# Optimization experiments

Measured on AMD Instinct MI355X. Metric: run time of the kernel, lower is better.

## Reference

```python
import jax, jax.numpy as jnp
import numpy as np

N = 3072      # packed vision tokens (multiple of _BLOCK=128, so no padding needed)
D = 1280      # hidden_size
H = 16        # num_heads
K = 80        # head_dim = D // H
NSEG = 8      # number of packed images/segments


def setup_inputs() -> dict:
    key = jax.random.key(0)
    ks = jax.random.split(key, 8)
    hidden_ND = jax.random.normal(ks[0], (N, D), jnp.float32)
    inner = jnp.sort(jax.random.randint(ks[1], (NSEG - 1,), 1, N)).astype(jnp.int32)
    cu_seqlens = jnp.concatenate([
        jnp.zeros((1,), jnp.int32), inner, jnp.full((1,), N, jnp.int32)])
    theta = jax.random.uniform(ks[2], (N, K), jnp.float32, 0.0, 2.0 * np.pi)
    cos_NK = jnp.cos(theta)
    sin_NK = jnp.sin(theta)
    sd = 1.0 / np.sqrt(D)  # lecun_normal-ish scale
    qkv_w = jax.random.normal(ks[3], (D, 3 * D), jnp.float32) * sd
    qkv_b = jax.random.normal(ks[4], (3 * D,), jnp.float32) * 0.01
    proj_w = jax.random.normal(ks[5], (D, D), jnp.float32) * sd
    proj_b = jax.random.normal(ks[6], (D,), jnp.float32) * 0.01
    return {"hidden_ND": hidden_ND, "cu_seqlens": cu_seqlens,
            "cos_NK": cos_NK, "sin_NK": sin_NK,
            "qkv_w": qkv_w, "qkv_b": qkv_b,
            "proj_w": proj_w, "proj_b": proj_b}


def _rotate_half(x):
    x1, x2 = jnp.split(x, 2, axis=-1)
    return jnp.concatenate([-x2, x1], axis=-1)


def _apply_vision_rope(q_NHK, k_NHK, cos_NK, sin_NK):
    c = cos_NK[:, None, :]  # (N, 1, K) broadcast over heads
    s = sin_NK[:, None, :]
    q = q_NHK * c + _rotate_half(q_NHK) * s
    k = k_NHK * c + _rotate_half(k_NHK) * s
    return q, k


def reference(hidden_ND, cu_seqlens, cos_NK, sin_NK, qkv_w, qkv_b, proj_w, proj_b):
    n = hidden_ND.shape[0]
    scale = K ** (-0.5)
    qkv = (hidden_ND @ qkv_w + qkv_b).reshape(n, 3, H, K)
    q_NHK, k_NHK, v_NHK = qkv[:, 0], qkv[:, 1], qkv[:, 2]
    q_NHK, k_NHK = _apply_vision_rope(q_NHK, k_NHK, cos_NK, sin_NK)

    # segment-boundary mask: token i attends to [k_start[i], k_end[i])
    idx = jnp.arange(n)
    seg = jnp.searchsorted(cu_seqlens[1:], idx, side='right')
    nseg = cu_seqlens.shape[0]
    k_start = cu_seqlens[jnp.minimum(seg, nseg - 2)]
    k_end = cu_seqlens[jnp.minimum(seg + 1, nseg - 1)]
    mask = (idx[None, :] >= k_start[:, None]) & (idx[None, :] < k_end[:, None])  # (Nq, Nk)

    scores = jnp.einsum('nhk,mhk->hnm', q_NHK, k_NHK) * scale  # (H, N, N)
    scores = jnp.where(mask[None], scores, jnp.float32(-1e30))
    probs = jax.nn.softmax(scores, axis=-1)
    attn = jnp.einsum('hnm,mhk->nhk', probs, v_NHK)  # (N, H, K)
    out_ND = attn.reshape(n, H * K) @ proj_w + proj_b
    return out_ND
```

## Files before the change

### kernel.cpp

```cpp
#include <hip/hip_runtime.h>

#define NTOK 3072
#define DM   1280
#define NH   16
#define HD   80
#define HDS  104
#define KVB  64
#define NSEG 8
#define QKVC 3840

typedef __attribute__((ext_vector_type(4))) float  f32x4;
typedef __attribute__((ext_vector_type(8))) __bf16 bf16x8;
typedef __attribute__((ext_vector_type(8))) unsigned short ushort8;
typedef __attribute__((ext_vector_type(4))) unsigned short ushort4v;
typedef __attribute__((ext_vector_type(2))) unsigned int  u32x2;

static __device__ __forceinline__ unsigned short f2bf(float f){
  union{float f; unsigned int u;} v; v.f=f;
  unsigned int r = v.u + 0x7fffu + ((v.u>>16)&1u);
  return (unsigned short)(r>>16);
}
static __device__ __forceinline__ float bf2f(unsigned short u){
  union{unsigned int i; float f;} v; v.i = ((unsigned int)u)<<16; return v.f;
}
static __device__ __forceinline__ void gload_lds16(const void* g, void* l){
  __builtin_amdgcn_global_load_lds((const __attribute__((address_space(1))) void*)g,
                                   (__attribute__((address_space(3))) void*)l, 16, 0, 0);
}

__global__ void cast_f32_bf16(const float* __restrict__ src, unsigned short* __restrict__ dst, int n){
  int i = (blockIdx.x*256 + threadIdx.x)*4;
  if (i >= n) return;
  f32x4 v = *reinterpret_cast<const f32x4*>(&src[i]);
  ushort4v o;
  o[0]=f2bf(v[0]); o[1]=f2bf(v[1]); o[2]=f2bf(v[2]); o[3]=f2bf(v[3]);
  *reinterpret_cast<ushort4v*>(&dst[i]) = o;
}

__global__ void transpose_cast(const float* __restrict__ src, unsigned short* __restrict__ dst, int R, int C){
  __shared__ unsigned short tile[32][33];
  int c0 = blockIdx.x*32, r0 = blockIdx.y*32;
  int tx = threadIdx.x, ty = threadIdx.y;
  #pragma unroll
  for (int i=0;i<4;i++){
    int r = r0 + ty + i*8;
    tile[ty+i*8][tx] = f2bf(src[(size_t)r*C + c0 + tx]);
  }
  __syncthreads();
  #pragma unroll
  for (int i=0;i<4;i++){
    int c = c0 + ty + i*8;
    dst[(size_t)c*R + r0 + tx] = tile[tx][ty+i*8];
  }
}

__global__ void transpose_v(const unsigned short* __restrict__ qkv, unsigned short* __restrict__ Vt){
  __shared__ unsigned short tile[32][33];
  int n0 = blockIdx.x*32, d0 = blockIdx.y*32, h = blockIdx.z;
  int tx = threadIdx.x, ty = threadIdx.y;
  #pragma unroll
  for (int i=0;i<4;i++){
    int n = n0 + ty + i*8;
    int d = d0 + tx;
    tile[ty+i*8][tx] = (d < HD) ? qkv[(size_t)n*QKVC + 2*DM + h*HD + d] : (unsigned short)0;
  }
  __syncthreads();
  #pragma unroll
  for (int i=0;i<4;i++){
    int d = d0 + ty + i*8;
    if (d < HD) Vt[((size_t)h*HD + d)*NTOK + n0 + tx] = tile[tx][ty+i*8];
  }
}

template<int OUT_BF16>
__global__ __launch_bounds__(256) void gemm_bt(
    const unsigned short* __restrict__ A,
    const unsigned short* __restrict__ Bt,
    const float* __restrict__ bias,
    unsigned short* __restrict__ Cb,
    float* __restrict__ Cf,
    int M, int Ncol, int Kd, int nbn)
{
  __shared__ unsigned short As[2][128*32];
  __shared__ unsigned short Bs[2][128*32];
  const int tid  = threadIdx.x;
  const int lane = tid & 63, wave = tid >> 6;
  const int wr = wave >> 1, wc = wave & 1;
  const int cpx = gridDim.x >> 3;
  const int id  = (blockIdx.x & 7)*cpx + (blockIdx.x >> 3);
  const int bm = id / nbn, bn = id % nbn;
  const f32x4 vzero = {0.f,0.f,0.f,0.f};

  f32x4 acc[4][4];
  #pragma unroll
  for (int i=0;i<4;i++)
    #pragma unroll
    for (int j=0;j<4;j++) acc[i][j] = vzero;

  const int rsub = lane>>2;
  const int kc   = (lane&3)*8;
  const unsigned short* Ab = A  + (size_t)(bm*128 + wave*32 + rsub)*Kd + kc;
  const unsigned short* Bb = Bt + (size_t)(bn*128 + wave*32 + rsub)*Kd + kc;

  #pragma unroll
  for (int i=0;i<2;i++){
    gload_lds16(Ab + (size_t)i*16*Kd, &As[0][(wave*2+i)*512]);
    gload_lds16(Bb + (size_t)i*16*Kd, &Bs[0][(wave*2+i)*512]);
  }
  __syncthreads();

  int cur = 0;
  for (int k0=32; k0<Kd; k0+=32){
    #pragma unroll
    for (int i=0;i<2;i++){
      gload_lds16(Ab + (size_t)i*16*Kd + k0, &As[cur^1][(wave*2+i)*512]);
      gload_lds16(Bb + (size_t)i*16*Kd + k0, &Bs[cur^1][(wave*2+i)*512]);
    }
    bf16x8 a[4], b[4];
    #pragma unroll
    for (int mf=0; mf<4; mf++)
      a[mf] = *reinterpret_cast<const bf16x8*>(&As[cur][(wr*64 + mf*16 + (lane&15))*32 + ((lane>>4)<<3)]);
    #pragma unroll
    for (int nf=0; nf<4; nf++)
      b[nf] = *reinterpret_cast<const bf16x8*>(&Bs[cur][(wc*64 + nf*16 + (lane&15))*32 + ((lane>>4)<<3)]);
    #pragma unroll
    for (int mf=0; mf<4; mf++)
      #pragma unroll
      for (int nf=0; nf<4; nf++)
        acc[mf][nf] = __builtin_amdgcn_mfma_f32_16x16x32_bf16(a[mf], b[nf], acc[mf][nf], 0,0,0);
    __syncthreads();
    cur ^= 1;
  }
  {
    bf16x8 a[4], b[4];
    #pragma unroll
    for (int mf=0; mf<4; mf++)
      a[mf] = *reinterpret_cast<const bf16x8*>(&As[cur][(wr*64 + mf*16 + (lane&15))*32 + ((lane>>4)<<3)]);
    #pragma unroll
    for (int nf=0; nf<4; nf++)
      b[nf] = *reinterpret_cast<const bf16x8*>(&Bs[cur][(wc*64 + nf*16 + (lane&15))*32 + ((lane>>4)<<3)]);
    #pragma unroll
    for (int mf=0; mf<4; mf++)
      #pragma unroll
      for (int nf=0; nf<4; nf++)
        acc[mf][nf] = __builtin_amdgcn_mfma_f32_16x16x32_bf16(a[mf], b[nf], acc[mf][nf], 0,0,0);
  }

  const int crow0 = bm*128 + wr*64;
  const int ccol0 = bn*128 + wc*64;
  #pragma unroll
  for (int nf=0; nf<4; nf++){
    int col = ccol0 + nf*16 + (lane&15);
    float bv = bias[col];
    #pragma unroll
    for (int mf=0; mf<4; mf++){
      #pragma unroll
      for (int r=0;r<4;r++){
        int row = crow0 + mf*16 + ((lane>>4)<<2) + r;
        float v = acc[mf][nf][r] + bv;
        if (OUT_BF16) Cb[(size_t)row*Ncol + col] = f2bf(v);
        else          Cf[(size_t)row*Ncol + col] = v;
      }
    }
  }
}

__global__ void rope_repack(const unsigned short* __restrict__ qkv,
                            const float* __restrict__ cosNK, const float* __restrict__ sinNK,
                            unsigned short* __restrict__ Qr, unsigned short* __restrict__ Kr)
{
  int idx = blockIdx.x*256 + threadIdx.x;
  if (idx >= NH*NTOK*HDS) return;
  int k  = idx % HDS;
  int nh = idx / HDS;
  int n  = nh % NTOK;
  int h  = nh / NTOK;
  size_t dsti = (size_t)(h*NTOK + n)*HDS + k;
  if (k >= HD){ Qr[dsti]=0; Kr[dsti]=0; return; }
  float c = cosNK[n*HD + k], s = sinNK[n*HD + k];
  int   kp  = (k < 40) ? (k+40) : (k-40);
  float sgn = (k < 40) ? -1.f : 1.f;
  size_t base = (size_t)n*QKVC + h*HD;
  float q   = bf2f(qkv[base + k]);
  float qp  = bf2f(qkv[base + kp]);
  float kk  = bf2f(qkv[base + DM + k]);
  float kkp = bf2f(qkv[base + DM + kp]);
  Qr[dsti] = f2bf(q*c  + sgn*qp*s);
  Kr[dsti] = f2bf(kk*c + sgn*kkp*s);
}

__global__ __launch_bounds__(256) void attn_kernel(
    const unsigned short* __restrict__ Qr,
    const unsigned short* __restrict__ Kr,
    const unsigned short* __restrict__ Vt,
    const int* __restrict__ cu,
    unsigned short* __restrict__ attn_out)
{
  __shared__ unsigned short Ps[64*KVB];

  const int h   = blockIdx.y;
  const int q0  = blockIdx.x*64;
  const int tid = threadIdx.x;
  const int lane = tid & 63, wave = tid >> 6;
  const int l16 = lane & 15, g16 = lane >> 4;
  const int qrow = q0 + wave*16 + l16;
  const f32x4 vzero = {0.f,0.f,0.f,0.f};

  int seg = 0, seg0 = 0, seg1 = 0;
  #pragma unroll
  for (int j=1;j<NSEG;j++){
    int c = cu[j];
    seg  += (c <= qrow)  ? 1 : 0;
    seg0 += (c <= q0)    ? 1 : 0;
    seg1 += (c <= q0+63) ? 1 : 0;
  }
  const int rst = cu[seg], ren = cu[seg+1];
  const int kmin = cu[seg0], kmax = cu[seg1+1];
  const int kt0 = kmin & ~(KVB-1);

  bf16x8 bq[3];
  {
    const unsigned short* qsrc = Qr + ((size_t)h*NTOK + qrow)*HDS;
    #pragma unroll
    for (int ds=0; ds<3; ds++)
      bq[ds] = *reinterpret_cast<const bf16x8*>(&qsrc[ds*32 + g16*8]);
  }

  f32x4 accO[5];
  #pragma unroll
  for (int i=0;i<5;i++) accO[i] = vzero;
  float m_r = -1e30f, l_r = 0.f;
  const float scale = 0.11180339887498948f;

  const int prow  = wave*16 + l16;
  char* const psb = (char*)Ps;
  const int pswz  = (prow & 7) << 4;

  for (int kt = kt0; kt < kmax; kt += KVB){
    ushort8 vreg[2][5];
    #pragma unroll
    for (int ks=0; ks<2; ks++)
      #pragma unroll
      for (int cf=0; cf<5; cf++)
        vreg[ks][cf] = *reinterpret_cast<const ushort8*>(
            &Vt[((size_t)h*HD + cf*16 + l16)*NTOK + kt + ks*32 + g16*8]);

    const unsigned short* ksrc = Kr + ((size_t)h*NTOK + kt)*HDS;
    f32x4 accST[4];
    #pragma unroll
    for (int i=0;i<4;i++) accST[i] = vzero;
    #pragma unroll
    for (int ds=0; ds<3; ds++){
      #pragma unroll
      for (int f=0; f<4; f++){
        bf16x8 ak = *reinterpret_cast<const bf16x8*>(&ksrc[(size_t)(f*16 + l16)*HDS + ds*32 + g16*8]);
        accST[f] = __builtin_amdgcn_mfma_f32_16x16x32_bf16(ak, bq[ds], accST[f], 0,0,0);
      }
    }

    float mx = -1e30f;
    #pragma unroll
    for (int f=0; f<4; f++){
      #pragma unroll
      for (int r=0; r<4; r++){
        int kcol = kt + f*16 + g16*4 + r;
        bool ok = (kcol >= rst) && (kcol < ren);
        float s = accST[f][r]*scale;
        accST[f][r] = ok ? s : -3e38f;
        mx = fmaxf(mx, accST[f][r]);
      }
    }
    mx = fmaxf(mx, __shfl_xor(mx, 16));
    mx = fmaxf(mx, __shfl_xor(mx, 32));
    const float mnew  = fmaxf(m_r, mx);
    const float alpha = __expf(m_r - mnew);
    m_r = mnew;
    float lsum = 0.f;
    #pragma unroll
    for (int f=0; f<4; f++){
      #pragma unroll
      for (int r=0; r<4; r++){
        float e = __expf(accST[f][r] - mnew);
        accST[f][r] = e;
        lsum += e;
      }
    }
    lsum += __shfl_xor(lsum, 16);
    lsum += __shfl_xor(lsum, 32);
    l_r = l_r*alpha + lsum;
    #pragma unroll
    for (int cf=0; cf<5; cf++) accO[cf] *= alpha;

    #pragma unroll
    for (int f=0; f<4; f++){
      u32x2 pk;
      pk[0] = (unsigned int)f2bf(accST[f][0]) | ((unsigned int)f2bf(accST[f][1]) << 16);
      pk[1] = (unsigned int)f2bf(accST[f][2]) | ((unsigned int)f2bf(accST[f][3]) << 16);
      *reinterpret_cast<u32x2*>(psb + ((prow*128 + f*32 + g16*8) ^ pswz)) = pk;
    }

    #pragma unroll
    for (int ks=0; ks<2; ks++){
      bf16x8 bp = *reinterpret_cast<const bf16x8*>(psb + ((prow*128 + ks*64 + g16*16) ^ pswz));
      #pragma unroll
      for (int cf=0; cf<5; cf++){
        bf16x8 av = __builtin_bit_cast(bf16x8, vreg[ks][cf]);
        accO[cf] = __builtin_amdgcn_mfma_f32_16x16x32_bf16(av, bp, accO[cf], 0,0,0);
      }
    }
  }

  const float inv = 1.f / l_r;
  #pragma unroll
  for (int cf=0; cf<5; cf++){
    ushort4v o;
    #pragma unroll
    for (int r=0;r<4;r++) o[r] = f2bf(accO[cf][r]*inv);
    *reinterpret_cast<ushort4v*>(&attn_out[(size_t)qrow*DM + h*HD + cf*16 + g16*4]) = o;
  }
}

extern "C" void kernel_launch(void* const* d_in, const int* in_sizes, int n_in,
                              void* d_out, int out_size, void* d_ws, size_t ws_size,
                              hipStream_t stream)
{
  const float* hidden = (const float*)d_in[0];
  const int*   cu     = (const int*)  d_in[1];
  const float* cosNK  = (const float*)d_in[2];
  const float* sinNK  = (const float*)d_in[3];
  const float* qkv_w  = (const float*)d_in[4];
  const float* qkv_b  = (const float*)d_in[5];
  const float* proj_w = (const float*)d_in[6];
  const float* proj_b = (const float*)d_in[7];
  float* out = (float*)d_out;

  char* w = (char*)d_ws;
  unsigned short* hid_bf  = (unsigned short*)w;  w += (size_t)NTOK*DM*2;
  unsigned short* qkvwT   = (unsigned short*)w;  w += (size_t)QKVC*DM*2;
  unsigned short* projwT  = (unsigned short*)w;  w += (size_t)DM*DM*2;
  unsigned short* qkv_bf  = (unsigned short*)w;  w += (size_t)NTOK*QKVC*2;
  unsigned short* Qr      = (unsigned short*)w;  w += (size_t)NH*NTOK*HDS*2;
  unsigned short* Kr      = (unsigned short*)w;  w += (size_t)NH*NTOK*HDS*2;
  unsigned short* Vt      = qkvwT;
  unsigned short* attn_bf = hid_bf;

  cast_f32_bf16<<<(NTOK*DM/4 + 255)/256, 256, 0, stream>>>(hidden, hid_bf, NTOK*DM);
  transpose_cast<<<dim3(QKVC/32, DM/32), dim3(32,8), 0, stream>>>(qkv_w, qkvwT, DM, QKVC);
  transpose_cast<<<dim3(DM/32,  DM/32), dim3(32,8), 0, stream>>>(proj_w, projwT, DM, DM);
  gemm_bt<1><<<dim3((NTOK/128)*(QKVC/128)), 256, 0, stream>>>(hid_bf, qkvwT, qkv_b, qkv_bf, nullptr, NTOK, QKVC, DM, QKVC/128);
  rope_repack<<<(NH*NTOK*HDS + 255)/256, 256, 0, stream>>>(qkv_bf, cosNK, sinNK, Qr, Kr);
  transpose_v<<<dim3(NTOK/32, 3, NH), dim3(32,8), 0, stream>>>(qkv_bf, Vt);
  attn_kernel<<<dim3(NTOK/64, NH), 256, 0, stream>>>(Qr, Kr, Vt, cu, attn_bf);
  gemm_bt<0><<<dim3((NTOK/128)*(DM/128)), 256, 0, stream>>>(attn_bf, projwT, proj_b, nullptr, out, NTOK, DM, DM, DM/128);
}
```

Baseline: 256.3 us.

## Vectorize RoPE repack, shrink head stride, and bound KV range per wave

The RoPE repack kernel now processes 8 elements per thread with 16-byte loads and stores instead of one scalar element per thread. The padded head stride drops from 104 to 96. The attention kernel computes the KV tile range per wave (16 rows) instead of per 64-row block, so waves skip KV tiles outside their own segments, and each wave gets its own shared-memory P region. This cuts redundant masked work near segment boundaries and rope overhead, at the cost of divergent loop trip counts across waves in a block.

```diff
diff --git a/kernel.cpp b/kernel.cpp
--- a/kernel.cpp
+++ b/kernel.cpp
@@ -4,7 +4,7 @@
 #define DM   1280
 #define NH   16
 #define HD   80
-#define HDS  104
+#define HDS  96
 #define KVB  64
 #define NSEG 8
 #define QKVC 3840
@@ -170,23 +170,41 @@
                             unsigned short* __restrict__ Qr, unsigned short* __restrict__ Kr)
 {
   int idx = blockIdx.x*256 + threadIdx.x;
-  if (idx >= NH*NTOK*HDS) return;
-  int k  = idx % HDS;
-  int nh = idx / HDS;
+  if (idx >= NH*NTOK*12) return;
+  int c  = idx % 12;
+  int nh = idx / 12;
   int n  = nh % NTOK;
   int h  = nh / NTOK;
-  size_t dsti = (size_t)(h*NTOK + n)*HDS + k;
-  if (k >= HD){ Qr[dsti]=0; Kr[dsti]=0; return; }
-  float c = cosNK[n*HD + k], s = sinNK[n*HD + k];
-  int   kp  = (k < 40) ? (k+40) : (k-40);
-  float sgn = (k < 40) ? -1.f : 1.f;
-  size_t base = (size_t)n*QKVC + h*HD;
-  float q   = bf2f(qkv[base + k]);
-  float qp  = bf2f(qkv[base + kp]);
-  float kk  = bf2f(qkv[base + DM + k]);
-  float kkp = bf2f(qkv[base + DM + kp]);
-  Qr[dsti] = f2bf(q*c  + sgn*qp*s);
-  Kr[dsti] = f2bf(kk*c + sgn*kkp*s);
+  unsigned short* qd = Qr + (size_t)(h*NTOK + n)*HDS + c*8;
+  unsigned short* kd = Kr + (size_t)(h*NTOK + n)*HDS + c*8;
+  if (c >= 10){
+    ushort8 z = {0,0,0,0,0,0,0,0};
+    *reinterpret_cast<ushort8*>(qd) = z;
+    *reinterpret_cast<ushort8*>(kd) = z;
+    return;
+  }
+  const int k0  = c*8;
+  const int kp0 = (k0 < 40) ? (k0+40) : (k0-40);
+  const float sgn = (k0 < 40) ? -1.f : 1.f;
+  const size_t base = (size_t)n*QKVC + h*HD;
+  ushort8 q  = *reinterpret_cast<const ushort8*>(&qkv[base + k0]);
+  ushort8 qp = *reinterpret_cast<const ushort8*>(&qkv[base + kp0]);
+  ushort8 kk = *reinterpret_cast<const ushort8*>(&qkv[base + DM + k0]);
+  ushort8 kp = *reinterpret_cast<const ushort8*>(&qkv[base + DM + kp0]);
+  f32x4 c0 = *reinterpret_cast<const f32x4*>(&cosNK[n*HD + k0]);
+  f32x4 c1 = *reinterpret_cast<const f32x4*>(&cosNK[n*HD + k0 + 4]);
+  f32x4 s0 = *reinterpret_cast<const f32x4*>(&sinNK[n*HD + k0]);
+  f32x4 s1 = *reinterpret_cast<const f32x4*>(&sinNK[n*HD + k0 + 4]);
+  ushort8 qo, ko;
+  #pragma unroll
+  for (int j=0;j<8;j++){
+    float cj = (j<4) ? c0[j] : c1[j-4];
+    float sj = (j<4) ? s0[j] : s1[j-4];
+    qo[j] = f2bf(bf2f(q[j])*cj  + sgn*bf2f(qp[j])*sj);
+    ko[j] = f2bf(bf2f(kk[j])*cj + sgn*bf2f(kp[j])*sj);
+  }
+  *reinterpret_cast<ushort8*>(qd) = qo;
+  *reinterpret_cast<ushort8*>(kd) = ko;
 }
 
 __global__ __launch_bounds__(256) void attn_kernel(
@@ -196,7 +214,7 @@
     const int* __restrict__ cu,
     unsigned short* __restrict__ attn_out)
 {
-  __shared__ unsigned short Ps[64*KVB];
+  __shared__ unsigned short Ps[4*16*KVB];
 
   const int h   = blockIdx.y;
   const int q0  = blockIdx.x*64;
@@ -206,17 +224,18 @@
   const int qrow = q0 + wave*16 + l16;
   const f32x4 vzero = {0.f,0.f,0.f,0.f};
 
-  int seg = 0, seg0 = 0, seg1 = 0;
+  const int rowA = q0 + wave*16, rowB = rowA + 15;
+  int seg = 0, sA = 0, sB = 0;
   #pragma unroll
   for (int j=1;j<NSEG;j++){
     int c = cu[j];
-    seg  += (c <= qrow)  ? 1 : 0;
-    seg0 += (c <= q0)    ? 1 : 0;
-    seg1 += (c <= q0+63) ? 1 : 0;
+    seg += (c <= qrow) ? 1 : 0;
+    sA  += (c <= rowA) ? 1 : 0;
+    sB  += (c <= rowB) ? 1 : 0;
   }
   const int rst = cu[seg], ren = cu[seg+1];
-  const int kmin = cu[seg0], kmax = cu[seg1+1];
-  const int kt0 = kmin & ~(KVB-1);
+  const int kminW = cu[sA], kmaxW = cu[sB+1];
+  const int kt0w = kminW & ~(KVB-1);
 
   bf16x8 bq[3];
   {
@@ -232,11 +251,10 @@
   float m_r = -1e30f, l_r = 0.f;
   const float scale = 0.11180339887498948f;
 
-  const int prow  = wave*16 + l16;
-  char* const psb = (char*)Ps;
-  const int pswz  = (prow & 7) << 4;
-
-  for (int kt = kt0; kt < kmax; kt += KVB){
+  char* const psb = (char*)Ps + wave*2048;
+  const int pswz  = (l16 & 7) << 4;
+
+  for (int kt = kt0w; kt < kmaxW; kt += KVB){
     ushort8 vreg[2][5];
     #pragma unroll
     for (int ks=0; ks<2; ks++)
@@ -296,12 +314,12 @@
       u32x2 pk;
       pk[0] = (unsigned int)f2bf(accST[f][0]) | ((unsigned int)f2bf(accST[f][1]) << 16);
       pk[1] = (unsigned int)f2bf(accST[f][2]) | ((unsigned int)f2bf(accST[f][3]) << 16);
-      *reinterpret_cast<u32x2*>(psb + ((prow*128 + f*32 + g16*8) ^ pswz)) = pk;
+      *reinterpret_cast<u32x2*>(psb + ((l16*128 + f*32 + g16*8) ^ pswz)) = pk;
     }
 
     #pragma unroll
     for (int ks=0; ks<2; ks++){
-      bf16x8 bp = *reinterpret_cast<const bf16x8*>(psb + ((prow*128 + ks*64 + g16*16) ^ pswz));
+      bf16x8 bp = *reinterpret_cast<const bf16x8*>(psb + ((l16*128 + ks*64 + g16*16) ^ pswz));
       #pragma unroll
       for (int cf=0; cf<5; cf++){
         bf16x8 av = __builtin_bit_cast(bf16x8, vreg[ks][cf]);
@@ -348,7 +366,7 @@
   transpose_cast<<<dim3(QKVC/32, DM/32), dim3(32,8), 0, stream>>>(qkv_w, qkvwT, DM, QKVC);
   transpose_cast<<<dim3(DM/32,  DM/32), dim3(32,8), 0, stream>>>(proj_w, projwT, DM, DM);
   gemm_bt<1><<<dim3((NTOK/128)*(QKVC/128)), 256, 0, stream>>>(hid_bf, qkvwT, qkv_b, qkv_bf, nullptr, NTOK, QKVC, DM, QKVC/128);
-  rope_repack<<<(NH*NTOK*HDS + 255)/256, 256, 0, stream>>>(qkv_bf, cosNK, sinNK, Qr, Kr);
+  rope_repack<<<(NH*NTOK*12 + 255)/256, 256, 0, stream>>>(qkv_bf, cosNK, sinNK, Qr, Kr);
   transpose_v<<<dim3(NTOK/32, 3, NH), dim3(32,8), 0, stream>>>(qkv_bf, Vt);
   attn_kernel<<<dim3(NTOK/64, NH), 256, 0, stream>>>(Qr, Kr, Vt, cu, attn_bf);
   gemm_bt<0><<<dim3((NTOK/128)*(DM/128)), 256, 0, stream>>>(attn_bf, projwT, proj_b, nullptr, out, NTOK, DM, DM, DM/128);
```

Result: no change. 255.9 us (-0.1%).
